# Kernel optimization log

Hardware: AMD Instinct MI355X
Metric: run time of the kernel (lower is better)

The kernel has to match this reference:

```python
import jax, jax.numpy as jnp
import numpy as np

B, N, DIM = 32, 1024, 512
HEADS, HEAD_DIM = 8, 64
MLP_HIDDEN = 2048
MAX_DIST = 7
TABLE_SIZE = (2 * MAX_DIST + 1) ** 2  # 225


def setup_inputs() -> dict:
    key = jax.random.key(0)
    ks = jax.random.split(key, 8)
    return {
        "x": jax.random.normal(ks[0], (B, N, DIM), jnp.float32),
        "qkv_w": jax.random.normal(ks[1], (3 * DIM, DIM), jnp.float32) * 0.02,
        "proj_w": jax.random.normal(ks[2], (DIM, DIM), jnp.float32) * 0.02,
        "proj_b": jnp.zeros((DIM,), jnp.float32),
        "mlp_w1": jax.random.normal(ks[3], (MLP_HIDDEN, DIM), jnp.float32) * 0.02,
        "mlp_b1": jnp.zeros((MLP_HIDDEN,), jnp.float32),
        "mlp_w2": jax.random.normal(ks[4], (DIM, MLP_HIDDEN), jnp.float32) * 0.02,
        "mlp_b2": jnp.zeros((DIM,), jnp.float32),
        "norm1_g": jnp.ones((DIM,), jnp.float32),
        "norm1_b": jnp.zeros((DIM,), jnp.float32),
        "norm2_g": jnp.ones((DIM,), jnp.float32),
        "norm2_b": jnp.zeros((DIM,), jnp.float32),
        "bias_table": jax.random.normal(ks[5], (TABLE_SIZE, HEADS), jnp.float32) * 0.02,
        "height": 32,
        "width": 32,
    }


def _rel_pos_index(height, width):
    # exact replication of RelativePositionBias index math (numpy, trace-time)
    coords = np.stack(np.meshgrid(np.arange(height), np.arange(width), indexing="ij"))  # [2,H,W]
    flat = coords.reshape(2, -1)                         # [2,N]
    rel = flat[:, :, None] - flat[:, None, :]            # [2,N,N]
    rel = rel.transpose(1, 2, 0).copy()                  # [N,N,2]
    rel[:, :, 0] += height - 1
    rel[:, :, 1] += width - 1
    rel[:, :, 0] *= 2 * width - 1
    idx = np.clip(rel.sum(-1), 0, TABLE_SIZE - 1)
    return jnp.asarray(idx, jnp.int32)                   # [N,N]


def _layernorm(x, g, b, eps=1e-5):
    mu = x.mean(-1, keepdims=True)
    var = ((x - mu) ** 2).mean(-1, keepdims=True)
    return (x - mu) * jax.lax.rsqrt(var + eps) * g + b


def reference(x, qkv_w, proj_w, proj_b, mlp_w1, mlp_b1, mlp_w2, mlp_b2,
              norm1_g, norm1_b, norm2_g, norm2_b, bias_table, height, width):
    scale = HEAD_DIM ** -0.5
    idx = _rel_pos_index(height, width)
    bias = bias_table[idx]                               # [N,N,heads]
    bias = jnp.transpose(bias, (2, 0, 1))                # [heads,N,N]

    shortcut = x
    h = _layernorm(x, norm1_g, norm1_b)
    qkv = h @ qkv_w.T                                    # [B,N,3*DIM]
    qkv = qkv.reshape(x.shape[0], x.shape[1], 3, HEADS, HEAD_DIM)
    qkv = jnp.transpose(qkv, (2, 0, 3, 1, 4))            # [3,B,h,N,d]
    q, k, v = qkv[0], qkv[1], qkv[2]
    attn = jnp.einsum("bhnd,bhmd->bhnm", q, k) * scale
    attn = attn + bias[None]
    attn = jax.nn.softmax(attn, axis=-1)
    o = jnp.einsum("bhnm,bhmd->bhnd", attn, v)           # [B,h,N,d]
    o = jnp.transpose(o, (0, 2, 1, 3)).reshape(x.shape)  # [B,N,DIM]
    o = o @ proj_w.T + proj_b
    x = shortcut + o

    shortcut = x
    h = _layernorm(x, norm2_g, norm2_b)
    h = jax.nn.gelu(h @ mlp_w1.T + mlp_b1, approximate=False)
    h = h @ mlp_w2.T + mlp_b2
    return shortcut + h
```

## Files before the change

### kernel.cpp

```cpp
#include <hip/hip_runtime.h>

typedef short bf16x8 __attribute__((ext_vector_type(8)));
typedef float f32x4 __attribute__((ext_vector_type(4)));
typedef unsigned short us8 __attribute__((ext_vector_type(8)));
typedef unsigned short us2 __attribute__((ext_vector_type(2)));

__device__ __forceinline__ float bf2f(unsigned short u) {
    union { unsigned i; float f; } v; v.i = ((unsigned)u) << 16; return v.f;
}
__device__ __forceinline__ unsigned short f2bf(float f) {
    union { float f; unsigned i; } v; v.f = f;
    unsigned r = v.i + 0x7fffu + ((v.i >> 16) & 1u);
    return (unsigned short)(r >> 16);
}
__device__ __forceinline__ float ldflex(const void* p, int isf32, long i) {
    return isf32 ? ((const float*)p)[i] : bf2f(((const unsigned short*)p)[i]);
}
__device__ __forceinline__ float gelu_exact(float v) {
    return 0.5f * v * (1.0f + erff(v * 0.70710678118654752f));
}
__device__ __forceinline__ us8 pack8u(const float* s) {
    us8 r;
    #pragma unroll
    for (int i = 0; i < 8; ++i) r[i] = f2bf(s[i]);
    return r;
}
__device__ __forceinline__ unsigned cvtpk_bf16(float lo, float hi) {
    unsigned u;
    asm("v_cvt_pk_bf16_f32 %0, %1, %2" : "=v"(u) : "v"(lo), "v"(hi));
    return u;
}

__device__ __forceinline__ void gld16(const void* g, void* l) {
    typedef __attribute__((address_space(1))) void GV;
    typedef __attribute__((address_space(3))) void LV;
    __builtin_amdgcn_global_load_lds((GV*)g, (LV*)l, 16, 0, 0);
}

struct SniffArgs { const void* p[13]; int n[13]; };

__global__ __launch_bounds__(64) void sniff_all(SniffArgs a, int* __restrict__ flags)
{
    const unsigned short* buf = (const unsigned short*)a.p[blockIdx.x];
    const int n_elems = a.n[blockIdx.x];
    __shared__ int cnt[3];
    if (threadIdx.x < 3) cnt[threadIdx.x] = 0;
    __syncthreads();
    int K = n_elems / 2; if (K > 1024) K = 1024; if (K < 1) K = 1;
    int ins = 0, ne = 0, no = 0;
    for (int i = threadIdx.x; i < K; i += 64) {
        const unsigned lo = buf[2 * i], hi = buf[2 * i + 1];
        const unsigned e = (lo >> 7) & 0xFF;
        ins += (lo != 0 && (e < 90 || e > 160)) ? 1 : 0;
        ne  += (lo != 0);
        no  += (hi != 0);
    }
    atomicAdd(&cnt[0], ins); atomicAdd(&cnt[1], ne); atomicAdd(&cnt[2], no);
    __syncthreads();
    if (threadIdx.x == 0)
        flags[blockIdx.x] = (cnt[0] * 10 > K) || (cnt[1] * 10 < K && cnt[2] * 2 > K);
}

struct CvtArgs { const void* src[7]; void* dst[7]; int fidx[7]; int n[7]; int tobf[7]; };

__global__ __launch_bounds__(256) void convert_params(CvtArgs a, const int* __restrict__ flags)
{
    const int t = blockIdx.y;
    const int i0 = (blockIdx.x * 256 + threadIdx.x) * 8;
    if (i0 >= a.n[t]) return;
    const int f = flags[a.fidx[t]];
    float v[8];
    if (f) {
        const float* s = (const float*)a.src[t] + i0;
        *(f32x4*)&v[0] = *(const f32x4*)s;
        *(f32x4*)&v[4] = *(const f32x4*)(s + 4);
    } else {
        us8 u = *(const us8*)((const unsigned short*)a.src[t] + i0);
        #pragma unroll
        for (int i = 0; i < 8; ++i) v[i] = bf2f(u[i]);
    }
    if (a.tobf[t]) {
        *(us8*)((unsigned short*)a.dst[t] + i0) = pack8u(v);
    } else {
        float* d = (float*)a.dst[t] + i0;
        *(f32x4*)d       = *(f32x4*)&v[0];
        *(f32x4*)(d + 4) = *(f32x4*)&v[4];
    }
}

__global__ __launch_bounds__(256) void gemm_bf16(
    const unsigned short* __restrict__ A, const unsigned short* __restrict__ W,
    void* __restrict__ C, int Nout, int K,
    const float* __restrict__ bias,
    const void* resid, const int* rflag, long resid_row0,
    int act, int out_bf16)
{
    __shared__ unsigned short As[2][128 * 32];
    __shared__ unsigned short Bs[2][128 * 32];
    const int tid  = threadIdx.x;
    const int lane = tid & 63, wv = tid >> 6;
    const int wrow = wv >> 1, wcol = wv & 1;
    const int fm = lane & 15, quad = lane >> 4;

    const int gx = gridDim.x;
    const int nwg = gx * gridDim.y;
    int lin = blockIdx.y * gx + blockIdx.x;
    lin = (lin & 7) * (nwg >> 3) + (lin >> 3);
    const int bm = (lin / gx) * 128, bn = (lin % gx) * 128;

    const int sr   = tid >> 2;
    const int sb   = (((tid & 3) ^ ((sr >> 1) & 3)) * 16);
    const char* Ab = (const char*)A;
    const char* Wb = (const char*)W;
    const long a0 = ((long)(bm + sr) * K) * 2 + sb;
    const long a1 = ((long)(bm + 64 + sr) * K) * 2 + sb;
    const long b0 = ((long)(bn + sr) * K) * 2 + sb;
    const long b1 = ((long)(bn + 64 + sr) * K) * 2 + sb;
    const int ld = tid * 16;

    auto stage = [&](int bsel, int k0b) {
        char* AD = (char*)As[bsel];
        char* BD = (char*)Bs[bsel];
        gld16(Ab + a0 + k0b, AD + ld);
        gld16(Ab + a1 + k0b, AD + 4096 + ld);
        gld16(Wb + b0 + k0b, BD + ld);
        gld16(Wb + b1 + k0b, BD + 4096 + ld);
    };

    f32x4 acc[4][4] = {};
    const int nt = (K * 2) / 64;

    const int xsw = (fm >> 1) & 3;

    stage(0, 0);
    stage(1, 64);
    int cur = 0;
    for (int t = 0; t < nt; ++t) {
        if (t + 1 < nt) { asm volatile("s_waitcnt vmcnt(4)" ::: "memory"); }
        else            { asm volatile("s_waitcnt vmcnt(0)" ::: "memory"); }
        __builtin_amdgcn_sched_barrier(0);
        __builtin_amdgcn_s_barrier();
        __builtin_amdgcn_sched_barrier(0);

        const unsigned short* Ac = As[cur];
        const unsigned short* Bc = Bs[cur];
        bf16x8 af[4], bw[4];
        #pragma unroll
        for (int u = 0; u < 4; ++u) {
            const int qs = (quad ^ xsw) * 8;
            af[u] = *(const bf16x8*)&Ac[(wrow * 64 + u * 16 + fm) * 32 + qs];
            bw[u] = *(const bf16x8*)&Bc[(wcol * 64 + u * 16 + fm) * 32 + qs];
        }
        __builtin_amdgcn_s_setprio(1);
        #pragma unroll
        for (int i = 0; i < 4; ++i)
            #pragma unroll
            for (int j = 0; j < 4; ++j)
                acc[i][j] = __builtin_amdgcn_mfma_f32_16x16x32_bf16(
                                af[i], bw[j], acc[i][j], 0, 0, 0);
        __builtin_amdgcn_s_setprio(0);

        asm volatile("s_waitcnt lgkmcnt(0)" ::: "memory");
        __builtin_amdgcn_sched_barrier(0);
        __builtin_amdgcn_s_barrier();
        __builtin_amdgcn_sched_barrier(0);
        if (t + 2 < nt) stage(cur, (t + 2) * 64);
        cur ^= 1;
    }

    const int crow0 = bm + wrow * 64, ccol0 = bn + wcol * 64;
    if (out_bf16) {
        unsigned short* Cb = (unsigned short*)C;
        #pragma unroll
        for (int j = 0; j < 4; ++j) {
            const int col = ccol0 + j * 16 + fm;
            const float bv = bias ? bias[col] : 0.0f;
            #pragma unroll
            for (int i = 0; i < 4; ++i)
                #pragma unroll
                for (int r = 0; r < 4; ++r) {
                    const int row = crow0 + i * 16 + quad * 4 + r;
                    float v = acc[i][j][r] + bv;
                    if (act) v = gelu_exact(v);
                    Cb[(long)row * Nout + col] = f2bf(v);
                }
        }
    } else {
        float* Cf = (float*)C;
        const int rfl = resid ? (rflag ? *rflag : 1) : 1;
        #pragma unroll
        for (int j = 0; j < 4; ++j) {
            const int col = ccol0 + j * 16 + fm;
            const float bv = bias ? bias[col] : 0.0f;
            #pragma unroll
            for (int i = 0; i < 4; ++i)
                #pragma unroll
                for (int r = 0; r < 4; ++r) {
                    const int row = crow0 + i * 16 + quad * 4 + r;
                    float v = acc[i][j][r] + bv;
                    if (act)   v = gelu_exact(v);
                    if (resid) v += ldflex(resid, rfl, (resid_row0 + row) * (long)Nout + col);
                    Cf[(long)row * Nout + col] = v;
                }
        }
    }
}

__global__ __launch_bounds__(256) void layernorm_512(
    const void* __restrict__ x, const int* __restrict__ xflag, long row0,
    const void* __restrict__ g, const int* __restrict__ gflag,
    const void* __restrict__ b, const int* __restrict__ bflag,
    unsigned short* __restrict__ o)
{
    const int row = blockIdx.x;
    const int tid = threadIdx.x;
    const int xf = xflag ? *xflag : 1;
    const long base = (row0 + row) * 512 + tid * 2;
    const float vx = ldflex(x, xf, base);
    const float vy = ldflex(x, xf, base + 1);
    float s  = vx + vy;
    float s2 = vx * vx + vy * vy;
    #pragma unroll
    for (int off = 32; off > 0; off >>= 1) {
        s  += __shfl_down(s, off);
        s2 += __shfl_down(s2, off);
    }
    __shared__ float ss[4], ss2[4];
    if ((tid & 63) == 0) { ss[tid >> 6] = s; ss2[tid >> 6] = s2; }
    __syncthreads();
    const float ts   = ss[0] + ss[1] + ss[2] + ss[3];
    const float ts2  = ss2[0] + ss2[1] + ss2[2] + ss2[3];
    const float mean = ts * (1.0f / 512.0f);
    const float var  = ts2 * (1.0f / 512.0f) - mean * mean;
    const float rstd = rsqrtf(var + 1e-5f);
    const int gf = *gflag, bff = *bflag;
    us2 r;
    r[0] = f2bf((vx - mean) * rstd * ldflex(g, gf, tid * 2)     + ldflex(b, bff, tid * 2));
    r[1] = f2bf((vy - mean) * rstd * ldflex(g, gf, tid * 2 + 1) + ldflex(b, bff, tid * 2 + 1));
    *(us2*)(o + (long)row * 512 + tid * 2) = r;
}

__global__ __launch_bounds__(256, 5) void attn_mfma(
    const unsigned short* __restrict__ qkv,
    const void* __restrict__ table, const int* __restrict__ tflag,
    unsigned short* __restrict__ o)
{
    __shared__ unsigned short Ks[512 * 8];
    __shared__ unsigned short Vt[64 * 72];
    __shared__ unsigned short Pl[4][16 * 72];
    __shared__ float Tbh[228];

    const int tid  = threadIdx.x;
    const int lane = tid & 63, wv = tid >> 6;
    const int fm = lane & 15, quad = lane >> 4;

    const int hw    = blockIdx.x + gridDim.x * (blockIdx.y + gridDim.y * blockIdx.z);
    const int total = gridDim.x * gridDim.y * gridDim.z;
    const int lin   = (hw & 7) * (total >> 3) + (hw >> 3);
    const int q0 = (lin & 15) * 64;
    const int h  = (lin >> 4) & 7;
    const int b  = lin >> 7;

    {
        const int tf = *tflag;
        if (tid < 228) {
            const int src = tid > 224 ? 224 : tid;
            Tbh[tid] = ldflex(table, tf, src * 8 + h);
        }
    }

    bf16x8 qa[2];
    {
        const unsigned short* qb = &qkv[(long)((b * 1024 + q0 + wv * 16 + fm) * 3) * 512
                                        + h * 64 + quad * 8];
        qa[0] = *(const bf16x8*)qb;
        qa[1] = *(const bf16x8*)(qb + 32);
    }

    const int qi0   = q0 + wv * 16 + quad * 4;
    const int base0 = 63 * (qi0 >> 5) + (qi0 & 31) + 1984;
    int idxr[4];
    #pragma unroll
    for (int c = 0; c < 4; ++c) {
        const int kj = c * 16 + fm;
        idxr[c] = base0 - (63 * (kj >> 5) + (kj & 31));
    }

    bf16x8 ones8;
    #pragma unroll
    for (int i = 0; i < 8; ++i) ones8[i] = (short)0x3F80;

    const int kc_fm   = tid & 15;
    const int kc_quad = (tid >> 4) & 3;
    const int kc_ch   = (tid >> 6) & 1;
    const int kc_c0   = (tid >> 7) & 1;
    const char* qkvB  = (const char*)qkv;
    long ksrc = (((long)(b * 1024 + kc_c0 * 16 + kc_fm) * 3 + 1) * 512
                 + h * 64 + kc_ch * 32 + kc_quad * 8) * 2;

    const int key_v = tid & 63;
    const int dv    = (tid >> 6) * 16;
    long vsrc = (((long)(b * 1024 + key_v) * 3 + 2) * 512 + h * 64 + dv) * 2;

    char* KsB = (char*)Ks;

    f32x4 acc[4] = {};
    f32x4 accS = {};
    float mrow[4] = {-1e30f, -1e30f, -1e30f, -1e30f};

    us8 kv0 = *(const us8*)(qkvB + ksrc);
    us8 kv1 = *(const us8*)(qkvB + ksrc + 98304);
    us8 vv0 = *(const us8*)(qkvB + vsrc);
    us8 vv1 = *(const us8*)(qkvB + vsrc + 16);

    for (int kt = 0; kt < 16; ++kt) {
        __syncthreads();

        *(us8*)(KsB + tid * 16)        = kv0;
        *(us8*)(KsB + 4096 + tid * 16) = kv1;
        #pragma unroll
        for (int i = 0; i < 8; ++i) Vt[(dv + i) * 72 + key_v]     = vv0[i];
        #pragma unroll
        for (int i = 0; i < 8; ++i) Vt[(dv + 8 + i) * 72 + key_v] = vv1[i];

        if (kt < 15) {
            ksrc += 196608; vsrc += 196608;
            kv0 = *(const us8*)(qkvB + ksrc);
            kv1 = *(const us8*)(qkvB + ksrc + 98304);
            vv0 = *(const us8*)(qkvB + vsrc);
            vv1 = *(const us8*)(qkvB + vsrc + 16);
        }

        asm volatile("s_waitcnt lgkmcnt(0)" ::: "memory");
        __builtin_amdgcn_s_barrier();

        f32x4 sv[4];
        __builtin_amdgcn_s_setprio(1);
        #pragma unroll
        for (int c = 0; c < 4; ++c) {
            f32x4 z = {};
            z = __builtin_amdgcn_mfma_f32_16x16x32_bf16(
                    qa[0], *(const bf16x8*)&Ks[(((c * 2 + 0) * 4 + quad) * 16 + fm) * 8],
                    z, 0, 0, 0);
            z = __builtin_amdgcn_mfma_f32_16x16x32_bf16(
                    qa[1], *(const bf16x8*)&Ks[(((c * 2 + 1) * 4 + quad) * 16 + fm) * 8],
                    z, 0, 0, 0);
            sv[c] = z;
        }
        __builtin_amdgcn_s_setprio(0);

        #pragma unroll
        for (int c = 0; c < 4; ++c) {
            const int i0 = idxr[c] > 224 ? 224 : idxr[c];
            const float* tb = &Tbh[i0];
            idxr[c] -= 126;
            #pragma unroll
            for (int r = 0; r < 4; ++r)
                sv[c][r] = fmaf(sv[c][r], 0.125f, tb[r]);
        }

        float alpha[4];
        #pragma unroll
        for (int r = 0; r < 4; ++r) {
            float mr = fmaxf(fmaxf(sv[0][r], sv[1][r]), fmaxf(sv[2][r], sv[3][r]));
            #pragma unroll
            for (int off = 1; off < 16; off <<= 1) mr = fmaxf(mr, __shfl_xor(mr, off));
            const float mnew = fmaxf(mrow[r], mr);
            alpha[r] = __expf(mrow[r] - mnew);
            mrow[r] = mnew;
            #pragma unroll
            for (int c = 0; c < 4; ++c)
                sv[c][r] = __expf(sv[c][r] - mnew);
        }

        unsigned short* Pw = Pl[wv];
        #pragma unroll
        for (int r = 0; r < 4; ++r) {
            const unsigned u01 = cvtpk_bf16(sv[0][r], sv[1][r]);
            const unsigned u23 = cvtpk_bf16(sv[2][r], sv[3][r]);
            const int row = (quad * 4 + r) * 72;
            Pw[row + fm]      = (unsigned short)u01;
            Pw[row + 16 + fm] = (unsigned short)(u01 >> 16);
            Pw[row + 32 + fm] = (unsigned short)u23;
            Pw[row + 48 + fm] = (unsigned short)(u23 >> 16);
        }

        const bf16x8 ap0 = *(const bf16x8*)&Pw[fm * 72 + quad * 8];
        const bf16x8 ap1 = *(const bf16x8*)&Pw[fm * 72 + 32 + quad * 8];
        __builtin_amdgcn_s_setprio(1);
        #pragma unroll
        for (int c = 0; c < 4; ++c) {
            #pragma unroll
            for (int r = 0; r < 4; ++r) acc[c][r] *= alpha[r];
            acc[c] = __builtin_amdgcn_mfma_f32_16x16x32_bf16(
                        ap0, *(const bf16x8*)&Vt[(c * 16 + fm) * 72 + quad * 8], acc[c], 0, 0, 0);
            acc[c] = __builtin_amdgcn_mfma_f32_16x16x32_bf16(
                        ap1, *(const bf16x8*)&Vt[(c * 16 + fm) * 72 + 32 + quad * 8], acc[c], 0, 0, 0);
        }
        #pragma unroll
        for (int r = 0; r < 4; ++r) accS[r] *= alpha[r];
        accS = __builtin_amdgcn_mfma_f32_16x16x32_bf16(ap0, ones8, accS, 0, 0, 0);
        accS = __builtin_amdgcn_mfma_f32_16x16x32_bf16(ap1, ones8, accS, 0, 0, 0);
        __builtin_amdgcn_s_setprio(0);
    }

    float rinv[4];
    #pragma unroll
    for (int r = 0; r < 4; ++r) rinv[r] = 1.0f / accS[r];
    #pragma unroll
    for (int r = 0; r < 4; ++r) {
        const long ob = (long)(b * 1024 + q0 + wv * 16 + quad * 4 + r) * 512 + h * 64;
        const unsigned u01 = cvtpk_bf16(acc[0][r] * rinv[r], acc[1][r] * rinv[r]);
        const unsigned u23 = cvtpk_bf16(acc[2][r] * rinv[r], acc[3][r] * rinv[r]);
        o[ob + fm]      = (unsigned short)u01;
        o[ob + 16 + fm] = (unsigned short)(u01 >> 16);
        o[ob + 32 + fm] = (unsigned short)u23;
        o[ob + 48 + fm] = (unsigned short)(u23 >> 16);
    }
}

extern "C" void kernel_launch(void* const* d_in, const int* in_sizes, int n_in,
                              void* d_out, int out_size, void* d_ws, size_t ws_size,
                              hipStream_t stream)
{
    (void)n_in; (void)out_size;
    float* out = (float*)d_out;

    constexpr int B = 32, N = 1024;

    int* flags = (int*)d_ws;
    {
        SniffArgs sa;
        for (int t = 0; t < 13; ++t) { sa.p[t] = d_in[t]; sa.n[t] = in_sizes[t]; }
        sniff_all<<<13, 64, 0, stream>>>(sa, flags);
    }

    unsigned short* Wq = (unsigned short*)((char*)d_ws + 256);
    unsigned short* Wp = Wq + 786432;
    unsigned short* W1 = Wp + 262144;
    unsigned short* W2 = W1 + 1048576;
    float* Bp = (float*)(W2 + 1048576);
    float* B1 = Bp + 512;
    float* B2 = B1 + 2048;
    char* scr = (char*)(B2 + 512);
    scr = (char*)(((size_t)scr + 255) & ~(size_t)255);

    {
        CvtArgs ca;
        ca.src[0] = d_in[1]; ca.dst[0] = Wq; ca.fidx[0] = 1; ca.n[0] = 786432;  ca.tobf[0] = 1;
        ca.src[1] = d_in[2]; ca.dst[1] = Wp; ca.fidx[1] = 2; ca.n[1] = 262144;  ca.tobf[1] = 1;
        ca.src[2] = d_in[4]; ca.dst[2] = W1; ca.fidx[2] = 4; ca.n[2] = 1048576; ca.tobf[2] = 1;
        ca.src[3] = d_in[6]; ca.dst[3] = W2; ca.fidx[3] = 6; ca.n[3] = 1048576; ca.tobf[3] = 1;
        ca.src[4] = d_in[3]; ca.dst[4] = Bp; ca.fidx[4] = 3; ca.n[4] = 512;     ca.tobf[4] = 0;
        ca.src[5] = d_in[5]; ca.dst[5] = B1; ca.fidx[5] = 5; ca.n[5] = 2048;    ca.tobf[5] = 0;
        ca.src[6] = d_in[7]; ca.dst[6] = B2; ca.fidx[6] = 7; ca.n[6] = 512;     ca.tobf[6] = 0;
        convert_params<<<dim3(512, 7), 256, 0, stream>>>(ca, flags);
    }

    const size_t fixed = (size_t)(scr - (char*)d_ws);
    const size_t per_batch = (size_t)N * 3072 * 2;
    int bpc = (int)((ws_size - fixed) / per_batch);
    if (bpc < 1) bpc = 1;
    if (bpc > B) bpc = B;

    unsigned short* Ln = (unsigned short*)scr;
    unsigned short* Hd = Ln + (size_t)bpc * N * 512;
    unsigned short* Ao = Hd + (size_t)bpc * N * 2048;

    for (int b0 = 0; b0 < B; b0 += bpc) {
        const int nb   = (B - b0) < bpc ? (B - b0) : bpc;
        const int rows = nb * N;
        const long r0  = (long)b0 * N;

        layernorm_512<<<rows, 256, 0, stream>>>(
            d_in[0], flags + 0, r0, d_in[8], flags + 8, d_in[9], flags + 9, Ln);
        gemm_bf16<<<dim3(12, rows / 128), 256, 0, stream>>>(
            Ln, Wq, Hd, 1536, 512, nullptr, nullptr, nullptr, 0, 0, 1);
        attn_mfma<<<dim3(16, 8, nb), 256, 0, stream>>>(
            Hd, d_in[12], flags + 12, Ao);
        gemm_bf16<<<dim3(4, rows / 128), 256, 0, stream>>>(
            Ao, Wp, out + r0 * 512, 512, 512,
            Bp, d_in[0], flags + 0, r0, 0, 0);
    }

    for (int b0 = 0; b0 < B; b0 += bpc) {
        const int nb   = (B - b0) < bpc ? (B - b0) : bpc;
        const int rows = nb * N;
        const long r0  = (long)b0 * N;

        layernorm_512<<<rows, 256, 0, stream>>>(
            out + r0 * 512, nullptr, 0, d_in[10], flags + 10, d_in[11], flags + 11, Ln);
        gemm_bf16<<<dim3(16, rows / 128), 256, 0, stream>>>(
            Ln, W1, Hd, 2048, 512, B1, nullptr, nullptr, 0, 1, 1);
        gemm_bf16<<<dim3(4, rows / 128), 256, 0, stream>>>(
            Hd, W2, out + r0 * 512, 512, 2048,
            B2, out + r0 * 512, nullptr, 0, 0, 0);
    }
}
```

Measured before the change: 854.3 us.

## Enlarge GEMM tiles to 256x256 with 8 waves per block

```diff
diff --git a/kernel.cpp b/kernel.cpp
--- a/kernel.cpp
+++ b/kernel.cpp
@@ -88,49 +88,51 @@
     }
 }
 
-__global__ __launch_bounds__(256) void gemm_bf16(
+__global__ __launch_bounds__(512, 2) void gemm_bf16_256(
     const unsigned short* __restrict__ A, const unsigned short* __restrict__ W,
     void* __restrict__ C, int Nout, int K,
     const float* __restrict__ bias,
     const void* resid, const int* rflag, long resid_row0,
     int act, int out_bf16)
 {
-    __shared__ unsigned short As[2][128 * 32];
-    __shared__ unsigned short Bs[2][128 * 32];
+    __shared__ unsigned short As[2][256 * 32];
+    __shared__ unsigned short Bs[2][256 * 32];
     const int tid  = threadIdx.x;
     const int lane = tid & 63, wv = tid >> 6;
-    const int wrow = wv >> 1, wcol = wv & 1;
+    const int wrow = wv >> 2, wcol = wv & 3;
     const int fm = lane & 15, quad = lane >> 4;
 
     const int gx = gridDim.x;
     const int nwg = gx * gridDim.y;
     int lin = blockIdx.y * gx + blockIdx.x;
     lin = (lin & 7) * (nwg >> 3) + (lin >> 3);
-    const int bm = (lin / gx) * 128, bn = (lin % gx) * 128;
-
-    const int sr   = tid >> 2;
-    const int sb   = (((tid & 3) ^ ((sr >> 1) & 3)) * 16);
+    const int bm = (lin / gx) * 256, bn = (lin % gx) * 256;
+
+    const long Kb = (long)K * 2;
+    const int srow  = tid >> 2;
+    const int sslot = (tid & 3) ^ ((tid >> 2) & 3) ^ ((tid >> 4) & 3);
     const char* Ab = (const char*)A;
     const char* Wb = (const char*)W;
-    const long a0 = ((long)(bm + sr) * K) * 2 + sb;
-    const long a1 = ((long)(bm + 64 + sr) * K) * 2 + sb;
-    const long b0 = ((long)(bn + sr) * K) * 2 + sb;
-    const long b1 = ((long)(bn + 64 + sr) * K) * 2 + sb;
+    const long a0 = (long)(bm + srow) * Kb + sslot * 16;
+    const long a1 = (long)(bm + 128 + srow) * Kb + sslot * 16;
+    const long b0 = (long)(bn + srow) * Kb + sslot * 16;
+    const long b1 = (long)(bn + 128 + srow) * Kb + sslot * 16;
     const int ld = tid * 16;
 
-    auto stage = [&](int bsel, int k0b) {
+    auto stage = [&](int bsel, long kb) {
         char* AD = (char*)As[bsel];
         char* BD = (char*)Bs[bsel];
-        gld16(Ab + a0 + k0b, AD + ld);
-        gld16(Ab + a1 + k0b, AD + 4096 + ld);
-        gld16(Wb + b0 + k0b, BD + ld);
-        gld16(Wb + b1 + k0b, BD + 4096 + ld);
+        gld16(Ab + a0 + kb, AD + ld);
+        gld16(Ab + a1 + kb, AD + 8192 + ld);
+        gld16(Wb + b0 + kb, BD + ld);
+        gld16(Wb + b1 + kb, BD + 8192 + ld);
     };
 
-    f32x4 acc[4][4] = {};
-    const int nt = (K * 2) / 64;
-
-    const int xsw = (fm >> 1) & 3;
+    const int rmix = (fm ^ (fm >> 2)) & 3;
+    const int rslot = ((quad ^ rmix) * 8);
+
+    f32x4 acc[8][4] = {};
+    const int nt = K / 32;
 
     stage(0, 0);
     stage(1, 64);
@@ -144,43 +146,39 @@
 
         const unsigned short* Ac = As[cur];
         const unsigned short* Bc = Bs[cur];
-        bf16x8 af[4], bw[4];
-        #pragma unroll
-        for (int u = 0; u < 4; ++u) {
-            const int qs = (quad ^ xsw) * 8;
-            af[u] = *(const bf16x8*)&Ac[(wrow * 64 + u * 16 + fm) * 32 + qs];
-            bw[u] = *(const bf16x8*)&Bc[(wcol * 64 + u * 16 + fm) * 32 + qs];
-        }
+        bf16x8 bwf[4];
+        #pragma unroll
+        for (int nf = 0; nf < 4; ++nf)
+            bwf[nf] = *(const bf16x8*)&Bc[(wcol * 64 + nf * 16 + fm) * 32 + rslot];
         __builtin_amdgcn_s_setprio(1);
         #pragma unroll
-        for (int i = 0; i < 4; ++i)
-            #pragma unroll
-            for (int j = 0; j < 4; ++j)
-                acc[i][j] = __builtin_amdgcn_mfma_f32_16x16x32_bf16(
-                                af[i], bw[j], acc[i][j], 0, 0, 0);
+        for (int mf = 0; mf < 8; ++mf) {
+            const bf16x8 af = *(const bf16x8*)&Ac[(wrow * 128 + mf * 16 + fm) * 32 + rslot];
+            #pragma unroll
+            for (int nf = 0; nf < 4; ++nf)
+                acc[mf][nf] = __builtin_amdgcn_mfma_f32_16x16x32_bf16(
+                                  af, bwf[nf], acc[mf][nf], 0, 0, 0);
+        }
         __builtin_amdgcn_s_setprio(0);
 
-        asm volatile("s_waitcnt lgkmcnt(0)" ::: "memory");
-        __builtin_amdgcn_sched_barrier(0);
         __builtin_amdgcn_s_barrier();
-        __builtin_amdgcn_sched_barrier(0);
-        if (t + 2 < nt) stage(cur, (t + 2) * 64);
+        if (t + 2 < nt) stage(cur, (long)(t + 2) * 64);
         cur ^= 1;
     }
 
-    const int crow0 = bm + wrow * 64, ccol0 = bn + wcol * 64;
+    const int crow0 = bm + wrow * 128, ccol0 = bn + wcol * 64;
     if (out_bf16) {
         unsigned short* Cb = (unsigned short*)C;
         #pragma unroll
-        for (int j = 0; j < 4; ++j) {
-            const int col = ccol0 + j * 16 + fm;
+        for (int nf = 0; nf < 4; ++nf) {
+            const int col = ccol0 + nf * 16 + fm;
             const float bv = bias ? bias[col] : 0.0f;
             #pragma unroll
-            for (int i = 0; i < 4; ++i)
+            for (int mf = 0; mf < 8; ++mf)
                 #pragma unroll
                 for (int r = 0; r < 4; ++r) {
-                    const int row = crow0 + i * 16 + quad * 4 + r;
-                    float v = acc[i][j][r] + bv;
+                    const int row = crow0 + mf * 16 + quad * 4 + r;
+                    float v = acc[mf][nf][r] + bv;
                     if (act) v = gelu_exact(v);
                     Cb[(long)row * Nout + col] = f2bf(v);
                 }
@@ -189,15 +187,15 @@
         float* Cf = (float*)C;
         const int rfl = resid ? (rflag ? *rflag : 1) : 1;
         #pragma unroll
-        for (int j = 0; j < 4; ++j) {
-            const int col = ccol0 + j * 16 + fm;
+        for (int nf = 0; nf < 4; ++nf) {
+            const int col = ccol0 + nf * 16 + fm;
             const float bv = bias ? bias[col] : 0.0f;
             #pragma unroll
-            for (int i = 0; i < 4; ++i)
+            for (int mf = 0; mf < 8; ++mf)
                 #pragma unroll
                 for (int r = 0; r < 4; ++r) {
-                    const int row = crow0 + i * 16 + quad * 4 + r;
-                    float v = acc[i][j][r] + bv;
+                    const int row = crow0 + mf * 16 + quad * 4 + r;
+                    float v = acc[mf][nf][r] + bv;
                     if (act)   v = gelu_exact(v);
                     if (resid) v += ldflex(resid, rfl, (resid_row0 + row) * (long)Nout + col);
                     Cf[(long)row * Nout + col] = v;
@@ -474,11 +472,11 @@
 
         layernorm_512<<<rows, 256, 0, stream>>>(
             d_in[0], flags + 0, r0, d_in[8], flags + 8, d_in[9], flags + 9, Ln);
-        gemm_bf16<<<dim3(12, rows / 128), 256, 0, stream>>>(
+        gemm_bf16_256<<<dim3(6, rows / 256), 512, 0, stream>>>(
             Ln, Wq, Hd, 1536, 512, nullptr, nullptr, nullptr, 0, 0, 1);
         attn_mfma<<<dim3(16, 8, nb), 256, 0, stream>>>(
             Hd, d_in[12], flags + 12, Ao);
-        gemm_bf16<<<dim3(4, rows / 128), 256, 0, stream>>>(
+        gemm_bf16_256<<<dim3(2, rows / 256), 512, 0, stream>>>(
             Ao, Wp, out + r0 * 512, 512, 512,
             Bp, d_in[0], flags + 0, r0, 0, 0);
     }
@@ -490,9 +488,9 @@
 
         layernorm_512<<<rows, 256, 0, stream>>>(
             out + r0 * 512, nullptr, 0, d_in[10], flags + 10, d_in[11], flags + 11, Ln);
-        gemm_bf16<<<dim3(16, rows / 128), 256, 0, stream>>>(
+        gemm_bf16_256<<<dim3(8, rows / 256), 512, 0, stream>>>(
             Ln, W1, Hd, 2048, 512, B1, nullptr, nullptr, 0, 1, 1);
-        gemm_bf16<<<dim3(4, rows / 128), 256, 0, stream>>>(
+        gemm_bf16_256<<<dim3(2, rows / 256), 512, 0, stream>>>(
             Hd, W2, out + r0 * 512, 512, 2048,
             B2, out + r0 * 512, nullptr, 0, 0, 0);
     }
```

Measured after the change: 1.010 ms. 1.18x slower.
